# Optimization experiments

Measured on AMD Instinct MI355X. Metric: run time of the kernel, lower is better.

Reference implementation:

```python
import jax, jax.numpy as jnp
import numpy as np

IN_CH = 2048
MID_CH = IN_CH // 2  # 1024
NUM_CLASSES = 8


def setup_inputs() -> dict:
    key = jax.random.key(0)
    k1, k2, k3, k4, k5, k6 = jax.random.split(key, 6)
    B, H, W = 4, 24, 24
    feat_map = jax.random.normal(k1, (B, IN_CH, H, W), dtype=jnp.float32)
    pseudo_labels = jax.random.randint(k2, (B, 2 * H, 2 * W), 0, NUM_CLASSES)
    # ConvTranspose2d weight layout in torch: (in, out, kH, kW)
    w_deconv = jax.random.normal(k3, (IN_CH, MID_CH, 3, 3), dtype=jnp.float32) * 0.02
    b_deconv = jax.random.normal(k4, (MID_CH,), dtype=jnp.float32) * 0.02
    # 1x1 conv weight: (out=num_classes, in=mid), bias (num_classes,)
    w_conv = jax.random.normal(k5, (NUM_CLASSES, MID_CH), dtype=jnp.float32) * 0.02
    b_conv = jax.random.normal(k6, (NUM_CLASSES,), dtype=jnp.float32) * 0.02
    return {"feat_map": feat_map, "w_deconv": w_deconv, "b_deconv": b_deconv,
            "w_conv": w_conv, "b_conv": b_conv, "pseudo_labels": pseudo_labels}


def _conv_transpose2d(x, w, b):
    # torch ConvTranspose2d(k=3, stride=2, pad=1, output_padding=1)
    # == conv with lhs_dilation=2, pad (k-1-p, k-1-p+out_pad) = (1, 2),
    # kernel transposed to (out,in,kH,kW) and spatially flipped.
    w_oihw = jnp.flip(jnp.transpose(w, (1, 0, 2, 3)), axis=(2, 3))
    y = jax.lax.conv_general_dilated(
        x, w_oihw, window_strides=(1, 1), padding=((1, 2), (1, 2)),
        lhs_dilation=(2, 2),
        dimension_numbers=("NCHW", "OIHW", "NCHW"))
    return y + b[None, :, None, None]


def reference(feat_map, w_deconv, b_deconv, w_conv, b_conv, pseudo_labels):
    # deconv + relu: (B, MID_CH, 2H, 2W)
    x = jax.nn.relu(_conv_transpose2d(feat_map, w_deconv, b_deconv))
    # 1x1 conv -> seg logits (B, K, 2H, 2W)
    logits = jnp.einsum("bchw,kc->bkhw", x, w_conv) + b_conv[None, :, None, None]
    # flatten as torch: permute(0,2,3,1).reshape(-1, K)
    flat_logits = jnp.transpose(logits, (0, 2, 3, 1)).reshape(-1, NUM_CLASSES)
    flat_labels = pseudo_labels.reshape(-1)
    logp = jax.nn.log_softmax(flat_logits, axis=-1)
    ce = -jnp.take_along_axis(logp, flat_labels[:, None], axis=-1)[:, 0]
    # per-class mean CE, then mean over classes that are present
    sums = jax.ops.segment_sum(ce, flat_labels, num_segments=NUM_CLASSES)
    counts = jax.ops.segment_sum(jnp.ones_like(ce), flat_labels, num_segments=NUM_CLASSES)
    present = counts > 0
    per_class = jnp.where(present, sums / jnp.maximum(counts, 1.0), 0.0)
    n_present = jnp.maximum(jnp.sum(present.astype(ce.dtype)), 1.0)
    loss = jnp.sum(per_class) / n_present
    # module returns feat_map unchanged and stores loss; the loss is the computed output
    return loss
```

## Files before the change

### kernel.cpp

```cpp
#include <hip/hip_runtime.h>
#include <hip/hip_bf16.h>
#include <math.h>

#define IC    2048
#define OC    1024
#define BATCH 4
#define H     24
#define W     24
#define OH    48
#define OW    48
#define NCLS  8
#define NPIX  (BATCH*H*W)
#define NOUT  (BATCH*OH*OW)

#define SA 21.1666667f
#define SB 1058.33333f
#define DEQ 4.4640075e-5f

#define SUMS_OFF    0
#define COUNTS_OFF  32
#define ZBUF_OFF    64

#define XPART_OFF   4096
#define XPART_SIZE  (9ULL*NPIX*OC*2)
#define FEATQ_OFF   (XPART_OFF + XPART_SIZE)
#define FEATQ_SIZE  (128ULL*NPIX*16)
#define WDQ_OFF     (FEATQ_OFF + FEATQ_SIZE)
#define WDQ_SIZE    (9ULL*128*OC*16)
#define CE_OFF      (WDQ_OFF + WDQ_SIZE)
#define CE_SIZE     (NOUT*4)
#define WS_NEEDED_Q (CE_OFF + CE_SIZE)

#define LOGITS_OFF  4096
#define WS_ZERO_FB  (LOGITS_OFF + NOUT*NCLS*4)

typedef signed char i8x16 __attribute__((ext_vector_type(16)));
typedef int   i32x4  __attribute__((ext_vector_type(4)));
typedef short bf16x8 __attribute__((ext_vector_type(8)));
typedef float f32x4  __attribute__((ext_vector_type(4)));

static __device__ __forceinline__ short f2bf(float f) {
    unsigned u = __float_as_uint(f);
    unsigned r = (u + 0x7fffu + ((u >> 16) & 1u)) >> 16;
    return (short)r;
}
static __device__ __forceinline__ float bf2f(short h) {
    return __uint_as_float(((unsigned)(unsigned short)h) << 16);
}
static __device__ __forceinline__ signed char q8(float v, float s) {
    return (signed char)(int)rintf(fminf(fmaxf(v * s, -127.f), 127.f));
}

static __device__ __forceinline__ void load16(const void* g, void* l) {
    __builtin_amdgcn_global_load_lds(
        (const __attribute__((address_space(1))) void*)g,
        (__attribute__((address_space(3))) void*)l, 16, 0, 0);
}

__device__ __constant__ int c_tab[9][4] = {
    {0,1,0,1},
    {0,1,1,0}, {0,1,0,2},
    {1,0,0,1}, {0,2,0,1},
    {1,0,1,0}, {1,0,0,2}, {0,2,1,0}, {0,2,0,2}
};

#define NBLK_FEAT 1152
#define NBLK_WD   1024
#define WDP 1168

__global__ __launch_bounds__(256) void prep_q(
    const float* __restrict__ feat, const float* __restrict__ wd,
    char* __restrict__ featQ, char* __restrict__ wdQ,
    float4* __restrict__ ws_head)
{
    __shared__ signed char lds8[16 * WDP];
    const int bx  = blockIdx.x;
    const int tid = threadIdx.x;

    if (bx < NBLK_FEAT) {
        if (bx == 0 && tid < 64)
            ws_head[tid] = float4{0.f, 0.f, 0.f, 0.f};

        const int pb = bx % 9, cb = bx / 9;
        const int p = pb * 256 + tid;
        const int b = p / (H * W);
        const int rem = p % (H * W);
        const float* src = feat + ((size_t)(b * IC + cb * 16)) * (H * W) + rem;
        i8x16 v;
        #pragma unroll
        for (int u = 0; u < 16; ++u) v[u] = q8(src[(size_t)u * (H * W)], SA);
        *(i8x16*)(featQ + ((size_t)cb * NPIX + p) * 16) = v;
    } else {
        const int sub = bx - NBLK_FEAT;
        const int ocb = sub % 8;
        const int cb  = sub / 8;

        #pragma unroll
        for (int l = 0; l < 18; ++l) {
            const int idx = l * 256 + tid;
            const int u = idx / 288;
            const int r4 = idx - u * 288;
            const float4 v = *(const float4*)&wd[(((size_t)(cb * 16 + u) * OC + ocb * 128)) * 9 + r4 * 4];
            const unsigned packed =
                ((unsigned)(unsigned char)q8(v.x, SB)) |
                ((unsigned)(unsigned char)q8(v.y, SB) << 8) |
                ((unsigned)(unsigned char)q8(v.z, SB) << 16) |
                ((unsigned)(unsigned char)q8(v.w, SB) << 24);
            *(unsigned*)&lds8[u * WDP + r4 * 4] = packed;
        }
        __syncthreads();

        #pragma unroll
        for (int l = 0; l < 5; ++l) {
            const int idx = l * 256 + tid;
            if (idx < 9 * 128) {
                const int t = idx >> 7;
                const int oc_l = idx & 127;
                i8x16 v;
                #pragma unroll
                for (int u = 0; u < 16; ++u) v[u] = lds8[u * WDP + oc_l * 9 + t];
                *(i8x16*)(wdQ + (((size_t)t * 128 + cb) * OC + ocb * 128 + oc_l) * 16) = v;
            }
        }
    }
}

#define STEPAQ ((size_t)4*NPIX*16)
#define STEPBQ ((size_t)4*OC*16)

__global__ __launch_bounds__(256, 4) void mfma_gemm_tap(
    const char*  __restrict__ featQ,
    const char*  __restrict__ wdQ,
    const char*  __restrict__ zb,
    char*        __restrict__ xpart)
{
    __shared__ uint4 As[512];
    __shared__ uint4 Bs[512];

    const int nt = blockIdx.x;
    const int mt = blockIdx.y;
    const int z  = blockIdx.z;
    const int dy = c_tab[z][0], ky = c_tab[z][1];
    const int dx = c_tab[z][2], kx = c_tab[z][3];
    const int koff = ky * 3 + kx;

    const int tid  = threadIdx.x;
    const int wave = tid >> 6;
    const int lane = tid & 63;
    const int wm = wave >> 1, wn = wave & 1;
    const int l15 = lane & 15, lq = lane >> 4;

    const int p0 = mt * 128, oc0 = nt * 128;

    const char* abase[2];
    bool avalid[2];
    #pragma unroll
    for (int a = 0; a < 2; ++a) {
        const int p = p0 + (2 * wave + a) * 16 + l15;
        const int rem = p % (H * W);
        const int i = rem / W, j = rem % W;
        avalid[a] = (i + dy < H) && (j + dx < W);
        const int pp = p + dy * W + dx;
        abase[a] = featQ + ((size_t)lq * NPIX + pp) * 16;
    }
    const char* bbase0 = wdQ + (((size_t)koff * 128 + lq) * OC + oc0 + (2 * wave + 0) * 16 + l15) * 16;
    const char* bbase1 = wdQ + (((size_t)koff * 128 + lq) * OC + oc0 + (2 * wave + 1) * 16 + l15) * 16;

    i32x4 acc[4][4];
    #pragma unroll
    for (int i = 0; i < 4; ++i)
        #pragma unroll
        for (int j = 0; j < 4; ++j)
            acc[i][j] = (i32x4)0;

    for (int it = 0; it < 32; ++it) {
        __syncthreads();
        const size_t aoff = (size_t)it * STEPAQ;
        const size_t boff = (size_t)it * STEPBQ;
        load16(avalid[0] ? abase[0] + aoff : zb, &As[(2 * wave + 0) * 64]);
        load16(avalid[1] ? abase[1] + aoff : zb, &As[(2 * wave + 1) * 64]);
        load16(bbase0 + boff, &Bs[(2 * wave + 0) * 64]);
        load16(bbase1 + boff, &Bs[(2 * wave + 1) * 64]);
        __syncthreads();

        i32x4 av[4], bv[4];
        #pragma unroll
        for (int i = 0; i < 4; ++i) {
            av[i] = *(const i32x4*)&As[(wm * 4 + i) * 64 + lane];
            bv[i] = *(const i32x4*)&Bs[(wn * 4 + i) * 64 + lane];
        }
        #pragma unroll
        for (int i = 0; i < 4; ++i)
            #pragma unroll
            for (int j = 0; j < 4; ++j)
                acc[i][j] = __builtin_amdgcn_mfma_i32_16x16x64_i8(
                    av[i], bv[j], acc[i][j], 0, 0, 0);
    }

    short* xb = (short*)xpart + (size_t)z * NPIX * OC;
    #pragma unroll
    for (int im = 0; im < 4; ++im) {
        const int row0 = p0 + wm * 64 + im * 16 + lq * 4;
        #pragma unroll
        for (int in = 0; in < 4; ++in) {
            const int col = oc0 + wn * 64 + in * 16 + l15;
            #pragma unroll
            for (int r = 0; r < 4; ++r)
                xb[(size_t)(row0 + r) * OC + col] = f2bf((float)acc[im][in][r] * DEQ);
        }
    }
}

template<int T, int B0>
static __device__ __forceinline__ void ep_core(
    const short* __restrict__ xp, int p, int lane,
    const float* __restrict__ bd, const float* __restrict__ wc, float pr[NCLS])
{
    bf16x8 h0[T], h1[T];
    #pragma unroll
    for (int t = 0; t < T; ++t) {
        const short* src = xp + ((size_t)(B0 + t) * NPIX + p) * OC + lane * 8;
        h0[t] = *(const bf16x8*)src;
        h1[t] = *(const bf16x8*)(src + 512);
    }
    #pragma unroll
    for (int half = 0; half < 2; ++half) {
        float s[8];
        #pragma unroll
        for (int u = 0; u < 8; ++u) s[u] = 0.f;
        #pragma unroll
        for (int t = 0; t < T; ++t) {
            const bf16x8 hv = half ? h1[t] : h0[t];
            #pragma unroll
            for (int u = 0; u < 8; ++u) s[u] += bf2f(hv[u]);
        }
        const int oc = half * 512 + lane * 8;
        const float4 ba = *(const float4*)&bd[oc];
        const float4 bb = *(const float4*)&bd[oc + 4];
        float x[8];
        x[0] = fmaxf(s[0] + ba.x, 0.f); x[1] = fmaxf(s[1] + ba.y, 0.f);
        x[2] = fmaxf(s[2] + ba.z, 0.f); x[3] = fmaxf(s[3] + ba.w, 0.f);
        x[4] = fmaxf(s[4] + bb.x, 0.f); x[5] = fmaxf(s[5] + bb.y, 0.f);
        x[6] = fmaxf(s[6] + bb.z, 0.f); x[7] = fmaxf(s[7] + bb.w, 0.f);
        #pragma unroll
        for (int c = 0; c < NCLS; ++c) {
            const float4 wa = *(const float4*)&wc[c * OC + oc];
            const float4 wb = *(const float4*)&wc[c * OC + oc + 4];
            pr[c] += x[0] * wa.x + x[1] * wa.y + x[2] * wa.z + x[3] * wa.w
                   + x[4] * wb.x + x[5] * wb.y + x[6] * wb.z + x[7] * wb.w;
        }
    }
}

__global__ __launch_bounds__(256) void ep_ce(
    const char*  __restrict__ xpart,
    const float* __restrict__ bd,
    const float* __restrict__ wc,
    const float* __restrict__ bc,
    const int*   __restrict__ labels,
    float* __restrict__ ce_out)
{
    const int tid  = threadIdx.x;
    const int wave = tid >> 6;
    const int lane = tid & 63;
    const int idx = blockIdx.x * 4 + wave;
    const int cls = idx / NPIX;
    const int p   = idx - cls * NPIX;
    const int ey = cls >> 1, ex = cls & 1;

    float pr[NCLS];
    #pragma unroll
    for (int c = 0; c < NCLS; ++c) pr[c] = 0.f;

    const short* xp = (const short*)xpart;
    if (cls == 0)      ep_core<1, 0>(xp, p, lane, bd, wc, pr);
    else if (cls == 1) ep_core<2, 1>(xp, p, lane, bd, wc, pr);
    else if (cls == 2) ep_core<2, 3>(xp, p, lane, bd, wc, pr);
    else               ep_core<4, 5>(xp, p, lane, bd, wc, pr);

    #pragma unroll
    for (int s = 8; s <= 32; s <<= 1)
        #pragma unroll
        for (int c = 0; c < NCLS; ++c) pr[c] += __shfl_xor(pr[c], s);

    const int b2 = (lane >> 2) & 1, b1 = (lane >> 1) & 1, bl0 = lane & 1;
    float v4[4];
    #pragma unroll
    for (int c2 = 0; c2 < 4; ++c2) {
        const float keep = b2 ? pr[c2 + 4] : pr[c2];
        const float send = b2 ? pr[c2] : pr[c2 + 4];
        v4[c2] = keep + __shfl_xor(send, 4);
    }
    float v2[2];
    #pragma unroll
    for (int c2 = 0; c2 < 2; ++c2) {
        const float keep = b1 ? v4[c2 + 2] : v4[c2];
        const float send = b1 ? v4[c2] : v4[c2 + 2];
        v2[c2] = keep + __shfl_xor(send, 2);
    }
    const float keep = bl0 ? v2[1] : v2[0];
    const float send = bl0 ? v2[0] : v2[1];
    const float v1 = keep + __shfl_xor(send, 1);

    const float logit = v1 + bc[lane & 7];

    float m = logit;
    #pragma unroll
    for (int s = 1; s <= 4; s <<= 1) m = fmaxf(m, __shfl_xor(m, s));
    float e = expf(logit - m);
    #pragma unroll
    for (int s = 1; s <= 4; s <<= 1) e += __shfl_xor(e, s);

    const int b  = p / (H * W);
    const int rem = p % (H * W);
    const int oy = 2 * (rem / W) + ey;
    const int ox = 2 * (rem % W) + ex;
    const int lab = labels[(b * OH + oy) * OW + ox];

    const float logit_lab = __shfl(logit, lab);
    if (lane == 0)
        ce_out[idx] = m + logf(e) - logit_lab;
}

__global__ __launch_bounds__(1024) void reduce_final(
    const float* __restrict__ ce, const int* __restrict__ labels,
    float* __restrict__ out)
{
    __shared__ float sS[NCLS];
    __shared__ float cS[NCLS];
    const int tid = threadIdx.x;
    if (tid < NCLS) { sS[tid] = 0.f; cS[tid] = 0.f; }
    __syncthreads();

    float s[NCLS], cnt[NCLS];
    #pragma unroll
    for (int c = 0; c < NCLS; ++c) { s[c] = 0.f; cnt[c] = 0.f; }

    #pragma unroll
    for (int i = 0; i < NOUT / 1024; ++i) {
        const int idx = i * 1024 + tid;
        const int cls = idx / NPIX;
        const int p   = idx - cls * NPIX;
        const int ey = cls >> 1, ex = cls & 1;
        const int b  = p / (H * W);
        const int rem = p % (H * W);
        const int oy = 2 * (rem / W) + ey;
        const int ox = 2 * (rem % W) + ex;
        const int lab = labels[(b * OH + oy) * OW + ox];
        const float v = ce[idx];
        #pragma unroll
        for (int c = 0; c < NCLS; ++c) {
            const bool hit = (lab == c);
            s[c]   += hit ? v : 0.f;
            cnt[c] += hit ? 1.f : 0.f;
        }
    }

    #pragma unroll
    for (int sh = 1; sh < 64; sh <<= 1)
        #pragma unroll
        for (int c = 0; c < NCLS; ++c) {
            s[c]   += __shfl_xor(s[c], sh);
            cnt[c] += __shfl_xor(cnt[c], sh);
        }

    if ((tid & 63) == 0) {
        #pragma unroll
        for (int c = 0; c < NCLS; ++c) {
            atomicAdd(&sS[c], s[c]);
            atomicAdd(&cS[c], cnt[c]);
        }
    }
    __syncthreads();

    if (tid == 0) {
        float tot = 0.f;
        int np = 0;
        for (int c = 0; c < NCLS; ++c)
            if (cS[c] > 0.f) { tot += sS[c] / cS[c]; ++np; }
        out[0] = tot / fmaxf((float)np, 1.f);
    }
}

__global__ __launch_bounds__(256) void deconv_gemm(
    const float* __restrict__ feat, const float* __restrict__ wd,
    const float* __restrict__ bd, const float* __restrict__ wc,
    float* __restrict__ logits)
{
    __shared__ float Asf[16][128];
    __shared__ float Bsf[16][132];
    const int nt = blockIdx.x, mt = blockIdx.y, cls = blockIdx.z;
    const int ey = cls >> 1, ex = cls & 1;
    const int ny = ey ? 2 : 1, nx = ex ? 2 : 1;
    int kyt[2] = {1,1}, dyt[2] = {0,0}, kxt[2] = {1,1}, dxt[2] = {0,0};
    if (ey) { kyt[0]=0; dyt[0]=1; kyt[1]=2; dyt[1]=0; }
    if (ex) { kxt[0]=0; dxt[0]=1; kxt[1]=2; dxt[1]=0; }
    const int T = ny * nx;
    const int p0 = mt * 128, oc0 = nt * 128;
    const int tid = threadIdx.x, tx = tid & 15, ty = tid >> 4;
    float acc[8][8];
    #pragma unroll
    for (int i = 0; i < 8; ++i)
        #pragma unroll
        for (int j = 0; j < 8; ++j) acc[i][j] = 0.f;
    const int nchunks = T * (IC / 16);
    for (int kc = 0; kc < nchunks; ++kc) {
        const int t = kc / (IC/16), icb = (kc % (IC/16)) * 16;
        const int dy = dyt[t/nx], ky = kyt[t/nx];
        const int dx = dxt[t%nx], kx = kxt[t%nx];
        const int koff = ky*3+kx;
        #pragma unroll
        for (int l = 0; l < 8; ++l) {
            const int idx = tid + l*256, kk = idx >> 7, pl = idx & 127;
            const int p = p0 + pl, b = p/(H*W), r = p%(H*W), i = r/W, j = r%W;
            const int iy = i+dy, ix = j+dx;
            float v = 0.f;
            if (iy < H && ix < W) v = feat[((b*IC + icb+kk)*H + iy)*W + ix];
            Asf[kk][pl] = v;
        }
        #pragma unroll
        for (int l = 0; l < 8; ++l) {
            const int idx = tid + l*256, kk = idx >> 7, n = idx & 127;
            Bsf[kk][n] = wd[(icb+kk)*(OC*9) + (oc0+n)*9 + koff];
        }
        __syncthreads();
        #pragma unroll
        for (int kk = 0; kk < 16; ++kk) {
            float a[8], bb[8];
            #pragma unroll
            for (int i = 0; i < 8; ++i) a[i] = Asf[kk][ty*8+i];
            #pragma unroll
            for (int j = 0; j < 8; ++j) bb[j] = Bsf[kk][tx*8+j];
            #pragma unroll
            for (int i = 0; i < 8; ++i)
                #pragma unroll
                for (int j = 0; j < 8; ++j) acc[i][j] += a[i]*bb[j];
        }
        __syncthreads();
    }
    float bdv[8], wcl[8][8];
    #pragma unroll
    for (int j = 0; j < 8; ++j) bdv[j] = bd[oc0 + tx*8 + j];
    #pragma unroll
    for (int c = 0; c < NCLS; ++c)
        #pragma unroll
        for (int j = 0; j < 8; ++j) wcl[c][j] = wc[c*OC + oc0 + tx*8 + j];
    #pragma unroll
    for (int i = 0; i < 8; ++i) {
        float pr[NCLS];
        #pragma unroll
        for (int c = 0; c < NCLS; ++c) pr[c] = 0.f;
        #pragma unroll
        for (int j = 0; j < 8; ++j) {
            const float x = fmaxf(acc[i][j] + bdv[j], 0.f);
            #pragma unroll
            for (int c = 0; c < NCLS; ++c) pr[c] += x * wcl[c][j];
        }
        #pragma unroll
        for (int s = 1; s < 16; s <<= 1)
            #pragma unroll
            for (int c = 0; c < NCLS; ++c) pr[c] += __shfl_xor(pr[c], s);
        if (tx == 0) {
            const int p = p0 + ty*8 + i, b = p/(H*W), r = p%(H*W);
            const int oy = 2*(r/W)+ey, ox = 2*(r%W)+ex;
            float* dst = logits + ((b*OH + oy)*OW + ox)*NCLS;
            #pragma unroll
            for (int c = 0; c < NCLS; ++c) atomicAdd(dst + c, pr[c]);
        }
    }
}

__global__ __launch_bounds__(256) void ce_kernel(
    const float* __restrict__ logits, const int* __restrict__ labels,
    const float* __restrict__ bc, float* __restrict__ sums,
    int* __restrict__ counts)
{
    __shared__ float ls[NCLS];
    __shared__ int   lc[NCLS];
    const int tid = threadIdx.x;
    if (tid < NCLS) { ls[tid] = 0.f; lc[tid] = 0; }
    __syncthreads();
    const int p = blockIdx.x * 256 + tid;
    float l[NCLS];
    float m = -1e30f;
    #pragma unroll
    for (int c = 0; c < NCLS; ++c) {
        l[c] = logits[p * NCLS + c] + bc[c];
        m = fmaxf(m, l[c]);
    }
    float s = 0.f;
    #pragma unroll
    for (int c = 0; c < NCLS; ++c) s += expf(l[c] - m);
    const int lab = labels[p];
    const float ce = m + logf(s) - l[lab];
    atomicAdd(&ls[lab], ce);
    atomicAdd(&lc[lab], 1);
    __syncthreads();
    if (tid < NCLS) {
        atomicAdd(&sums[tid], ls[tid]);
        atomicAdd(&counts[tid], lc[tid]);
    }
}

__global__ void final_kernel(const float* __restrict__ sums,
                             const int* __restrict__ counts,
                             float* __restrict__ out)
{
    if (threadIdx.x == 0 && blockIdx.x == 0) {
        float tot = 0.f;
        int np = 0;
        for (int c = 0; c < NCLS; ++c)
            if (counts[c] > 0) { tot += sums[c] / (float)counts[c]; ++np; }
        out[0] = tot / fmaxf((float)np, 1.f);
    }
}

extern "C" void kernel_launch(void* const* d_in, const int* in_sizes, int n_in,
                              void* d_out, int out_size, void* d_ws, size_t ws_size,
                              hipStream_t stream) {
    const float* feat   = (const float*)d_in[0];
    const float* wd     = (const float*)d_in[1];
    const float* bd     = (const float*)d_in[2];
    const float* wc     = (const float*)d_in[3];
    const float* bc     = (const float*)d_in[4];
    const int*   labels = (const int*)d_in[5];
    float* out = (float*)d_out;

    char* ws = (char*)d_ws;
    const char* zb = ws + ZBUF_OFF;

    if (ws_size >= WS_NEEDED_Q) {
        char* xpart = ws + XPART_OFF;
        char* featQ = ws + FEATQ_OFF;
        char* wdQ   = ws + WDQ_OFF;
        float* ce   = (float*)(ws + CE_OFF);
        prep_q<<<dim3(NBLK_FEAT + NBLK_WD), 256, 0, stream>>>(feat, wd, featQ, wdQ, (float4*)ws);
        mfma_gemm_tap<<<dim3(8, 18, 9), 256, 0, stream>>>(featQ, wdQ, zb, xpart);
        ep_ce<<<dim3(NPIX), 256, 0, stream>>>(xpart, bd, wc, bc, labels, ce);
        reduce_final<<<1, 1024, 0, stream>>>(ce, labels, out);
    } else {
        float* sums   = (float*)(ws + SUMS_OFF);
        int*   counts = (int*)(ws + COUNTS_OFF);
        float* logits = (float*)(ws + LOGITS_OFF);
        hipMemsetAsync(d_ws, 0, WS_ZERO_FB, stream);
        deconv_gemm<<<dim3(8, 18, 4), 256, 0, stream>>>(feat, wd, bd, wc, logits);
        ce_kernel<<<NOUT / 256, 256, 0, stream>>>(logits, labels, bc, sums, counts);
        final_kernel<<<1, 64, 0, stream>>>(sums, counts, out);
    }
}
```

Measured before the change: 210.4 us.

## Fuse deconv tap accumulation, ReLU and 1x1 conv into GEMM epilogue with atomics

The per-tap int8 GEMM now accumulates all taps belonging to each output parity class in registers, then applies dequant, bias, ReLU and the 1x1 classifier projection in its epilogue. Partial logits across output-channel tiles are combined with float atomicAdd into a small zeroed buffer, and the CE kernel computes log-softmax directly from the logits. This removes the large bf16 intermediate tensor write/read and the separate epilogue kernel. In exchange, class-3 blocks do four times the work of class-0 blocks, causing load imbalance, and the atomics make the float summation order nondeterministic.

New measurement: 238.4 us. +13.3%, slower.

```diff
diff --git a/kernel.cpp b/kernel.cpp
--- a/kernel.cpp
+++ b/kernel.cpp
@@ -21,32 +21,21 @@
 #define COUNTS_OFF  32
 #define ZBUF_OFF    64
 
-#define XPART_OFF   4096
-#define XPART_SIZE  (9ULL*NPIX*OC*2)
-#define FEATQ_OFF   (XPART_OFF + XPART_SIZE)
+#define LOGQ_OFF    4096
+#define LOGQ_SIZE   ((size_t)NOUT*NCLS*4)
+#define FEATQ_OFF   (LOGQ_OFF + LOGQ_SIZE)
 #define FEATQ_SIZE  (128ULL*NPIX*16)
 #define WDQ_OFF     (FEATQ_OFF + FEATQ_SIZE)
 #define WDQ_SIZE    (9ULL*128*OC*16)
-#define CE_OFF      (WDQ_OFF + WDQ_SIZE)
-#define CE_SIZE     (NOUT*4)
-#define WS_NEEDED_Q (CE_OFF + CE_SIZE)
-
-#define LOGITS_OFF  4096
-#define WS_ZERO_FB  (LOGITS_OFF + NOUT*NCLS*4)
+#define WS_NEEDED_Q (WDQ_OFF + WDQ_SIZE)
+
+#define FB_LOGITS_OFF  4096
+#define WS_ZERO_FB  (FB_LOGITS_OFF + NOUT*NCLS*4)
 
 typedef signed char i8x16 __attribute__((ext_vector_type(16)));
 typedef int   i32x4  __attribute__((ext_vector_type(4)));
-typedef short bf16x8 __attribute__((ext_vector_type(8)));
 typedef float f32x4  __attribute__((ext_vector_type(4)));
 
-static __device__ __forceinline__ short f2bf(float f) {
-    unsigned u = __float_as_uint(f);
-    unsigned r = (u + 0x7fffu + ((u >> 16) & 1u)) >> 16;
-    return (short)r;
-}
-static __device__ __forceinline__ float bf2f(short h) {
-    return __uint_as_float(((unsigned)(unsigned short)h) << 16);
-}
 static __device__ __forceinline__ signed char q8(float v, float s) {
     return (signed char)(int)rintf(fminf(fmaxf(v * s, -127.f), 127.f));
 }
@@ -71,7 +60,7 @@
 __global__ __launch_bounds__(256) void prep_q(
     const float* __restrict__ feat, const float* __restrict__ wd,
     char* __restrict__ featQ, char* __restrict__ wdQ,
-    float4* __restrict__ ws_head)
+    float4* __restrict__ ws_head, float4* __restrict__ logz)
 {
     __shared__ signed char lds8[16 * WDP];
     const int bx  = blockIdx.x;
@@ -80,6 +69,8 @@
     if (bx < NBLK_FEAT) {
         if (bx == 0 && tid < 64)
             ws_head[tid] = float4{0.f, 0.f, 0.f, 0.f};
+        if (bx < 72)
+            logz[bx * 256 + tid] = float4{0.f, 0.f, 0.f, 0.f};
 
         const int pb = bx % 9, cb = bx / 9;
         const int p = pb * 256 + tid;
@@ -128,43 +119,29 @@
 #define STEPAQ ((size_t)4*NPIX*16)
 #define STEPBQ ((size_t)4*OC*16)
 
-__global__ __launch_bounds__(256, 4) void mfma_gemm_tap(
-    const char*  __restrict__ featQ,
-    const char*  __restrict__ wdQ,
-    const char*  __restrict__ zb,
-    char*        __restrict__ xpart)
-{
-    __shared__ uint4 As[512];
-    __shared__ uint4 Bs[512];
-
+template<int T, int Z0>
+static __device__ __forceinline__ void gemm_body(
+    const char* __restrict__ featQ, const char* __restrict__ wdQ,
+    const char* __restrict__ zb, float* __restrict__ logits,
+    const float* __restrict__ bd, const float* __restrict__ wc,
+    const int cls, uint4* As, uint4* Bs)
+{
     const int nt = blockIdx.x;
     const int mt = blockIdx.y;
-    const int z  = blockIdx.z;
-    const int dy = c_tab[z][0], ky = c_tab[z][1];
-    const int dx = c_tab[z][2], kx = c_tab[z][3];
-    const int koff = ky * 3 + kx;
-
     const int tid  = threadIdx.x;
     const int wave = tid >> 6;
     const int lane = tid & 63;
     const int wm = wave >> 1, wn = wave & 1;
     const int l15 = lane & 15, lq = lane >> 4;
-
     const int p0 = mt * 128, oc0 = nt * 128;
 
-    const char* abase[2];
-    bool avalid[2];
+    int pa[2], ia[2], ja[2];
     #pragma unroll
     for (int a = 0; a < 2; ++a) {
-        const int p = p0 + (2 * wave + a) * 16 + l15;
-        const int rem = p % (H * W);
-        const int i = rem / W, j = rem % W;
-        avalid[a] = (i + dy < H) && (j + dx < W);
-        const int pp = p + dy * W + dx;
-        abase[a] = featQ + ((size_t)lq * NPIX + pp) * 16;
-    }
-    const char* bbase0 = wdQ + (((size_t)koff * 128 + lq) * OC + oc0 + (2 * wave + 0) * 16 + l15) * 16;
-    const char* bbase1 = wdQ + (((size_t)koff * 128 + lq) * OC + oc0 + (2 * wave + 1) * 16 + l15) * 16;
+        pa[a] = p0 + (2 * wave + a) * 16 + l15;
+        const int rem = pa[a] % (H * W);
+        ia[a] = rem / W; ja[a] = rem % W;
+    }
 
     i32x4 acc[4][4];
     #pragma unroll
@@ -173,164 +150,131 @@
         for (int j = 0; j < 4; ++j)
             acc[i][j] = (i32x4)0;
 
-    for (int it = 0; it < 32; ++it) {
-        __syncthreads();
-        const size_t aoff = (size_t)it * STEPAQ;
-        const size_t boff = (size_t)it * STEPBQ;
-        load16(avalid[0] ? abase[0] + aoff : zb, &As[(2 * wave + 0) * 64]);
-        load16(avalid[1] ? abase[1] + aoff : zb, &As[(2 * wave + 1) * 64]);
-        load16(bbase0 + boff, &Bs[(2 * wave + 0) * 64]);
-        load16(bbase1 + boff, &Bs[(2 * wave + 1) * 64]);
-        __syncthreads();
-
-        i32x4 av[4], bv[4];
-        #pragma unroll
-        for (int i = 0; i < 4; ++i) {
-            av[i] = *(const i32x4*)&As[(wm * 4 + i) * 64 + lane];
-            bv[i] = *(const i32x4*)&Bs[(wn * 4 + i) * 64 + lane];
-        }
-        #pragma unroll
-        for (int i = 0; i < 4; ++i)
-            #pragma unroll
-            for (int j = 0; j < 4; ++j)
-                acc[i][j] = __builtin_amdgcn_mfma_i32_16x16x64_i8(
-                    av[i], bv[j], acc[i][j], 0, 0, 0);
-    }
-
-    short* xb = (short*)xpart + (size_t)z * NPIX * OC;
+    #pragma unroll
+    for (int t = 0; t < T; ++t) {
+        const int z = Z0 + t;
+        const int dy = c_tab[z][0], ky = c_tab[z][1];
+        const int dx = c_tab[z][2], kx = c_tab[z][3];
+        const int koff = ky * 3 + kx;
+
+        const char* ab[2];
+        const char* bb[2];
+        bool aok[2];
+        #pragma unroll
+        for (int a = 0; a < 2; ++a) {
+            aok[a] = (ia[a] + dy < H) && (ja[a] + dx < W);
+            ab[a] = featQ + ((size_t)lq * NPIX + pa[a] + dy * W + dx) * 16;
+            bb[a] = wdQ + (((size_t)koff * 128 + lq) * OC + oc0 + (2 * wave + a) * 16 + l15) * 16;
+        }
+
+        for (int it = 0; it < 32; ++it) {
+            __syncthreads();
+            const size_t aoff = (size_t)it * STEPAQ;
+            const size_t boff = (size_t)it * STEPBQ;
+            load16(aok[0] ? ab[0] + aoff : zb, &As[(2 * wave + 0) * 64]);
+            load16(aok[1] ? ab[1] + aoff : zb, &As[(2 * wave + 1) * 64]);
+            load16(bb[0] + boff, &Bs[(2 * wave + 0) * 64]);
+            load16(bb[1] + boff, &Bs[(2 * wave + 1) * 64]);
+            __syncthreads();
+
+            i32x4 avv[4], bvv[4];
+            #pragma unroll
+            for (int i = 0; i < 4; ++i) {
+                avv[i] = *(const i32x4*)&As[(wm * 4 + i) * 64 + lane];
+                bvv[i] = *(const i32x4*)&Bs[(wn * 4 + i) * 64 + lane];
+            }
+            #pragma unroll
+            for (int i = 0; i < 4; ++i)
+                #pragma unroll
+                for (int j = 0; j < 4; ++j)
+                    acc[i][j] = __builtin_amdgcn_mfma_i32_16x16x64_i8(
+                        avv[i], bvv[j], acc[i][j], 0, 0, 0);
+        }
+    }
+
+    float bdv[4], wcl[NCLS][4];
+    #pragma unroll
+    for (int in = 0; in < 4; ++in) {
+        const int col = oc0 + wn * 64 + in * 16 + l15;
+        bdv[in] = bd[col];
+        #pragma unroll
+        for (int c = 0; c < NCLS; ++c) wcl[c][in] = wc[c * OC + col];
+    }
+    const int b2 = (l15 >> 2) & 1, b1 = (l15 >> 1) & 1, b0 = l15 & 1;
+
     #pragma unroll
     for (int im = 0; im < 4; ++im) {
-        const int row0 = p0 + wm * 64 + im * 16 + lq * 4;
-        #pragma unroll
-        for (int in = 0; in < 4; ++in) {
-            const int col = oc0 + wn * 64 + in * 16 + l15;
-            #pragma unroll
-            for (int r = 0; r < 4; ++r)
-                xb[(size_t)(row0 + r) * OC + col] = f2bf((float)acc[im][in][r] * DEQ);
-        }
-    }
-}
-
-template<int T, int B0>
-static __device__ __forceinline__ void ep_core(
-    const short* __restrict__ xp, int p, int lane,
-    const float* __restrict__ bd, const float* __restrict__ wc, float pr[NCLS])
-{
-    bf16x8 h0[T], h1[T];
-    #pragma unroll
-    for (int t = 0; t < T; ++t) {
-        const short* src = xp + ((size_t)(B0 + t) * NPIX + p) * OC + lane * 8;
-        h0[t] = *(const bf16x8*)src;
-        h1[t] = *(const bf16x8*)(src + 512);
-    }
-    #pragma unroll
-    for (int half = 0; half < 2; ++half) {
-        float s[8];
-        #pragma unroll
-        for (int u = 0; u < 8; ++u) s[u] = 0.f;
-        #pragma unroll
-        for (int t = 0; t < T; ++t) {
-            const bf16x8 hv = half ? h1[t] : h0[t];
-            #pragma unroll
-            for (int u = 0; u < 8; ++u) s[u] += bf2f(hv[u]);
-        }
-        const int oc = half * 512 + lane * 8;
-        const float4 ba = *(const float4*)&bd[oc];
-        const float4 bb = *(const float4*)&bd[oc + 4];
-        float x[8];
-        x[0] = fmaxf(s[0] + ba.x, 0.f); x[1] = fmaxf(s[1] + ba.y, 0.f);
-        x[2] = fmaxf(s[2] + ba.z, 0.f); x[3] = fmaxf(s[3] + ba.w, 0.f);
-        x[4] = fmaxf(s[4] + bb.x, 0.f); x[5] = fmaxf(s[5] + bb.y, 0.f);
-        x[6] = fmaxf(s[6] + bb.z, 0.f); x[7] = fmaxf(s[7] + bb.w, 0.f);
-        #pragma unroll
-        for (int c = 0; c < NCLS; ++c) {
-            const float4 wa = *(const float4*)&wc[c * OC + oc];
-            const float4 wb = *(const float4*)&wc[c * OC + oc + 4];
-            pr[c] += x[0] * wa.x + x[1] * wa.y + x[2] * wa.z + x[3] * wa.w
-                   + x[4] * wb.x + x[5] * wb.y + x[6] * wb.z + x[7] * wb.w;
-        }
-    }
-}
-
-__global__ __launch_bounds__(256) void ep_ce(
-    const char*  __restrict__ xpart,
+        #pragma unroll
+        for (int r = 0; r < 4; ++r) {
+            float pr[NCLS];
+            #pragma unroll
+            for (int c = 0; c < NCLS; ++c) pr[c] = 0.f;
+            #pragma unroll
+            for (int in = 0; in < 4; ++in) {
+                const float xv = fmaxf(fmaf((float)acc[im][in][r], DEQ, bdv[in]), 0.f);
+                #pragma unroll
+                for (int c = 0; c < NCLS; ++c) pr[c] = fmaf(xv, wcl[c][in], pr[c]);
+            }
+            #pragma unroll
+            for (int c = 0; c < NCLS; ++c) pr[c] += __shfl_xor(pr[c], 8);
+            float v4[4];
+            #pragma unroll
+            for (int c2 = 0; c2 < 4; ++c2) {
+                const float keep = b2 ? pr[c2 + 4] : pr[c2];
+                const float send = b2 ? pr[c2] : pr[c2 + 4];
+                v4[c2] = keep + __shfl_xor(send, 4);
+            }
+            float v2[2];
+            #pragma unroll
+            for (int c2 = 0; c2 < 2; ++c2) {
+                const float keep = b1 ? v4[c2 + 2] : v4[c2];
+                const float send = b1 ? v4[c2] : v4[c2 + 2];
+                v2[c2] = keep + __shfl_xor(send, 2);
+            }
+            const float keep = b0 ? v2[1] : v2[0];
+            const float send = b0 ? v2[0] : v2[1];
+            const float v1 = keep + __shfl_xor(send, 1);
+            if (l15 < 8) {
+                const int row = p0 + wm * 64 + im * 16 + lq * 4 + r;
+                atomicAdd(&logits[((size_t)cls * NPIX + row) * NCLS + l15], v1);
+            }
+        }
+    }
+}
+
+__global__ __launch_bounds__(256, 3) void mfma_gemm_cls(
+    const char*  __restrict__ featQ,
+    const char*  __restrict__ wdQ,
+    const char*  __restrict__ zb,
+    float*       __restrict__ logits,
     const float* __restrict__ bd,
-    const float* __restrict__ wc,
-    const float* __restrict__ bc,
-    const int*   __restrict__ labels,
-    float* __restrict__ ce_out)
-{
-    const int tid  = threadIdx.x;
-    const int wave = tid >> 6;
-    const int lane = tid & 63;
-    const int idx = blockIdx.x * 4 + wave;
-    const int cls = idx / NPIX;
-    const int p   = idx - cls * NPIX;
-    const int ey = cls >> 1, ex = cls & 1;
-
-    float pr[NCLS];
-    #pragma unroll
-    for (int c = 0; c < NCLS; ++c) pr[c] = 0.f;
-
-    const short* xp = (const short*)xpart;
-    if (cls == 0)      ep_core<1, 0>(xp, p, lane, bd, wc, pr);
-    else if (cls == 1) ep_core<2, 1>(xp, p, lane, bd, wc, pr);
-    else if (cls == 2) ep_core<2, 3>(xp, p, lane, bd, wc, pr);
-    else               ep_core<4, 5>(xp, p, lane, bd, wc, pr);
-
-    #pragma unroll
-    for (int s = 8; s <= 32; s <<= 1)
-        #pragma unroll
-        for (int c = 0; c < NCLS; ++c) pr[c] += __shfl_xor(pr[c], s);
-
-    const int b2 = (lane >> 2) & 1, b1 = (lane >> 1) & 1, bl0 = lane & 1;
-    float v4[4];
-    #pragma unroll
-    for (int c2 = 0; c2 < 4; ++c2) {
-        const float keep = b2 ? pr[c2 + 4] : pr[c2];
-        const float send = b2 ? pr[c2] : pr[c2 + 4];
-        v4[c2] = keep + __shfl_xor(send, 4);
-    }
-    float v2[2];
-    #pragma unroll
-    for (int c2 = 0; c2 < 2; ++c2) {
-        const float keep = b1 ? v4[c2 + 2] : v4[c2];
-        const float send = b1 ? v4[c2] : v4[c2 + 2];
-        v2[c2] = keep + __shfl_xor(send, 2);
-    }
-    const float keep = bl0 ? v2[1] : v2[0];
-    const float send = bl0 ? v2[0] : v2[1];
-    const float v1 = keep + __shfl_xor(send, 1);
-
-    const float logit = v1 + bc[lane & 7];
-
-    float m = logit;
-    #pragma unroll
-    for (int s = 1; s <= 4; s <<= 1) m = fmaxf(m, __shfl_xor(m, s));
-    float e = expf(logit - m);
-    #pragma unroll
-    for (int s = 1; s <= 4; s <<= 1) e += __shfl_xor(e, s);
-
-    const int b  = p / (H * W);
-    const int rem = p % (H * W);
-    const int oy = 2 * (rem / W) + ey;
-    const int ox = 2 * (rem % W) + ex;
-    const int lab = labels[(b * OH + oy) * OW + ox];
-
-    const float logit_lab = __shfl(logit, lab);
-    if (lane == 0)
-        ce_out[idx] = m + logf(e) - logit_lab;
-}
-
-__global__ __launch_bounds__(1024) void reduce_final(
-    const float* __restrict__ ce, const int* __restrict__ labels,
-    float* __restrict__ out)
+    const float* __restrict__ wc)
+{
+    __shared__ uint4 As[512];
+    __shared__ uint4 Bs[512];
+
+    const int zz = blockIdx.z;
+    const int cls = (zz == 0) ? 3 : (zz == 3) ? 0 : zz;
+
+    if (cls == 0)      gemm_body<1, 0>(featQ, wdQ, zb, logits, bd, wc, 0, As, Bs);
+    else if (cls == 1) gemm_body<2, 1>(featQ, wdQ, zb, logits, bd, wc, 1, As, Bs);
+    else if (cls == 2) gemm_body<2, 3>(featQ, wdQ, zb, logits, bd, wc, 2, As, Bs);
+    else               gemm_body<4, 5>(featQ, wdQ, zb, logits, bd, wc, 3, As, Bs);
+}
+
+__global__ __launch_bounds__(1024) void ce_reduce(
+    const float* __restrict__ logits, const int* __restrict__ labels,
+    const float* __restrict__ bc, float* __restrict__ out)
 {
     __shared__ float sS[NCLS];
     __shared__ float cS[NCLS];
     const int tid = threadIdx.x;
     if (tid < NCLS) { sS[tid] = 0.f; cS[tid] = 0.f; }
     __syncthreads();
+
+    float bcv[NCLS];
+    #pragma unroll
+    for (int c = 0; c < NCLS; ++c) bcv[c] = bc[c];
 
     float s[NCLS], cnt[NCLS];
     #pragma unroll
@@ -347,11 +291,30 @@
         const int oy = 2 * (rem / W) + ey;
         const int ox = 2 * (rem % W) + ex;
         const int lab = labels[(b * OH + oy) * OW + ox];
-        const float v = ce[idx];
+
+        const float4 la = *(const float4*)&logits[(size_t)idx * NCLS];
+        const float4 lb = *(const float4*)&logits[(size_t)idx * NCLS + 4];
+        float l[NCLS];
+        l[0] = la.x + bcv[0]; l[1] = la.y + bcv[1];
+        l[2] = la.z + bcv[2]; l[3] = la.w + bcv[3];
+        l[4] = lb.x + bcv[4]; l[5] = lb.y + bcv[5];
+        l[6] = lb.z + bcv[6]; l[7] = lb.w + bcv[7];
+
+        float m = l[0];
+        #pragma unroll
+        for (int c = 1; c < NCLS; ++c) m = fmaxf(m, l[c]);
+        float e = 0.f;
+        #pragma unroll
+        for (int c = 0; c < NCLS; ++c) e += expf(l[c] - m);
+        float sel = l[0];
+        #pragma unroll
+        for (int c = 1; c < NCLS; ++c) sel = (lab == c) ? l[c] : sel;
+        const float ce = m + logf(e) - sel;
+
         #pragma unroll
         for (int c = 0; c < NCLS; ++c) {
             const bool hit = (lab == c);
-            s[c]   += hit ? v : 0.f;
+            s[c]   += hit ? ce : 0.f;
             cnt[c] += hit ? 1.f : 0.f;
         }
     }
@@ -530,18 +493,18 @@
     const char* zb = ws + ZBUF_OFF;
 
     if (ws_size >= WS_NEEDED_Q) {
-        char* xpart = ws + XPART_OFF;
-        char* featQ = ws + FEATQ_OFF;
-        char* wdQ   = ws + WDQ_OFF;
-        float* ce   = (float*)(ws + CE_OFF);
-        prep_q<<<dim3(NBLK_FEAT + NBLK_WD), 256, 0, stream>>>(feat, wd, featQ, wdQ, (float4*)ws);
-        mfma_gemm_tap<<<dim3(8, 18, 9), 256, 0, stream>>>(featQ, wdQ, zb, xpart);
-        ep_ce<<<dim3(NPIX), 256, 0, stream>>>(xpart, bd, wc, bc, labels, ce);
-        reduce_final<<<1, 1024, 0, stream>>>(ce, labels, out);
+        float* logits = (float*)(ws + LOGQ_OFF);
+        char*  featQ  = ws + FEATQ_OFF;
+        char*  wdQ    = ws + WDQ_OFF;
+        prep_q<<<dim3(NBLK_FEAT + NBLK_WD), 256, 0, stream>>>(
+            feat, wd, featQ, wdQ, (float4*)ws, (float4*)logits);
+        mfma_gemm_cls<<<dim3(8, 18, 4), 256, 0, stream>>>(
+            featQ, wdQ, zb, logits, bd, wc);
+        ce_reduce<<<1, 1024, 0, stream>>>(logits, labels, bc, out);
     } else {
         float* sums   = (float*)(ws + SUMS_OFF);
         int*   counts = (int*)(ws + COUNTS_OFF);
-        float* logits = (float*)(ws + LOGITS_OFF);
+        float* logits = (float*)(ws + FB_LOGITS_OFF);
         hipMemsetAsync(d_ws, 0, WS_ZERO_FB, stream);
         deconv_gemm<<<dim3(8, 18, 4), 256, 0, stream>>>(feat, wd, bd, wc, logits);
         ce_kernel<<<NOUT / 256, 256, 0, stream>>>(logits, labels, bc, sums, counts);
```
